# Optimization experiments

Hardware: AMD Instinct MI355X
Metric: run time of the kernel (lower is better)

## Reference

```python
import jax, jax.numpy as jnp
import numpy as np


def conv1x1(x, w, b):
    # x: [B, Cin, D, H, W], w: [Cout, Cin], b: [Cout]
    return jnp.einsum('bcdhw,oc->bodhw', x, w) + b[None, :, None, None, None]


def setup_inputs() -> dict:
    key = jax.random.key(0)
    ks = jax.random.split(key, 9)
    B, C, D, H, W = 2, 64, 16, 16, 16
    Cc = 64          # context_dim
    C8 = C // 8      # inner attention dim
    s = 0.05
    return {
        'x': jax.random.normal(ks[0], (B, C, D, H, W), jnp.float32),
        'context': jax.random.normal(ks[1], (B, Cc, D, H, W), jnp.float32),
        'Wq': jax.random.normal(ks[2], (C8, C), jnp.float32) * s,
        'bq': jax.random.normal(ks[3], (C8,), jnp.float32) * s,
        'Wk': jax.random.normal(ks[4], (C8, Cc), jnp.float32) * s,
        'bk': jax.random.normal(ks[5], (C8,), jnp.float32) * s,
        'Wv': jax.random.normal(ks[6], (C, Cc), jnp.float32) * s,
        'bv': jax.random.normal(ks[7], (C,), jnp.float32) * s,
        'gamma': jax.random.normal(ks[8], (1,), jnp.float32) * s,
    }


def reference(x, context, Wq, bq, Wk, bk, Wv, bv, gamma):
    B, C, D, H, W = x.shape
    N = D * H * W
    q = conv1x1(x, Wq, bq).reshape(B, -1, N)        # [B, C/8, N]
    k = conv1x1(context, Wk, bk).reshape(B, -1, N)  # [B, C/8, N]
    v = conv1x1(context, Wv, bv).reshape(B, C, N)   # [B, C, N]
    # energy[b, n, m] = q[:, :, n] . k[:, :, m]  (no scaling, as in source)
    energy = jnp.einsum('bcn,bcm->bnm', q, k)       # [B, N, N]
    attn = jax.nn.softmax(energy, axis=-1)
    # out = v @ attn^T : out[b, c, n] = sum_m v[b, c, m] * attn[b, n, m]
    out = jnp.einsum('bcm,bnm->bcn', v, attn).reshape(B, C, D, H, W)
    return gamma[0] * out + x
```

## Files before the change

kernel.cpp:

```cpp
#include <hip/hip_runtime.h>

#define NTOK 4096

typedef __attribute__((ext_vector_type(8))) short short8;
typedef __attribute__((ext_vector_type(4))) float f32x4;
typedef __attribute__((ext_vector_type(4))) unsigned int uint4v;

__device__ __forceinline__ unsigned short f2bf(float f) {
    unsigned u = __float_as_uint(f);
    u += 0x7fffu + ((u >> 16) & 1u);
    return (unsigned short)(u >> 16);
}

__device__ __forceinline__ float bf2f(unsigned short h) {
    return __uint_as_float((unsigned)h << 16);
}

__device__ __forceinline__ unsigned int pk2(float lo, float hi) {
    return __builtin_amdgcn_perm(__float_as_uint(hi), __float_as_uint(lo), 0x07060302u);
}

__global__ __launch_bounds__(256) void proj(
    const float* __restrict__ x, const float* __restrict__ ctx,
    const float* __restrict__ Wq, const float* __restrict__ bq,
    const float* __restrict__ Wk, const float* __restrict__ bk,
    const float* __restrict__ Wv, const float* __restrict__ bv,
    unsigned short* __restrict__ qbf, unsigned short* __restrict__ kbf,
    unsigned short* __restrict__ vtp)
{
    __shared__ float sW[16 * 64];
    __shared__ float sB[16];
    int tid  = threadIdx.x;
    int ogrp = blockIdx.z;
    int b    = blockIdx.y;
    int n0   = blockIdx.x * 64;

    if (ogrp == 0) {
        for (int i = tid; i < 1024; i += 256)
            sW[i] = (i < 512) ? Wq[i] : Wk[i - 512];
        if (tid < 16) sB[tid] = (tid < 8) ? bq[tid] : bk[tid - 8];
    } else {
        for (int i = tid; i < 1024; i += 256)
            sW[i] = Wv[(ogrp - 1) * 1024 + i];
        if (tid < 16) sB[tid] = bv[(ogrp - 1) * 16 + tid];
    }
    __syncthreads();

    int nn   = tid & 63;
    int osub = tid >> 6;
    const float* inp = (ogrp == 0 && osub < 2) ? x : ctx;
    const float* ip  = inp + (size_t)b * 64 * NTOK + n0 + nn;

    float a0 = sB[osub * 4 + 0], a1 = sB[osub * 4 + 1];
    float a2 = sB[osub * 4 + 2], a3 = sB[osub * 4 + 3];
#pragma unroll 16
    for (int c = 0; c < 64; ++c) {
        float val = ip[(size_t)c * NTOK];
        a0 += sW[(osub * 4 + 0) * 64 + c] * val;
        a1 += sW[(osub * 4 + 1) * 64 + c] * val;
        a2 += sW[(osub * 4 + 2) * 64 + c] * val;
        a3 += sW[(osub * 4 + 3) * 64 + c] * val;
    }
    float av[4] = {a0, a1, a2, a3};

    if (ogrp == 0) {
        bool isq = osub < 2;
        float sc = isq ? 1.4426950408889634f : 1.0f;
        unsigned short* dst = isq ? qbf : kbf;
        int half = osub & 1;
        ushort4 pk = {f2bf(av[0] * sc), f2bf(av[1] * sc), f2bf(av[2] * sc), f2bf(av[3] * sc)};
        *(ushort4*)&dst[((size_t)b * NTOK + n0 + nn) * 8 + half * 4] = pk;
    } else {
        int cbase = (ogrp - 1) * 16 + osub * 4;
        int m   = n0 + nn;
        int T   = m >> 5;
        int mm  = m & 31;
        int p   = ((mm >> 2) & 3) * 8 + (mm >> 4) * 4 + (mm & 3);
        int qd  = p >> 3, j2 = p & 7;
        int ctv = cbase >> 4;
        unsigned short* vB = vtp + (size_t)b * 64 * NTOK
                           + ((size_t)T * 4 + ctv) * 512;
#pragma unroll
        for (int jj = 0; jj < 4; ++jj) {
            int lanev = ((cbase + jj) & 15) + 16 * qd;
            vB[lanev * 8 + j2] = f2bf(av[jj]);
        }
    }
}

__global__ __launch_bounds__(256, 2) void attn8(
    const unsigned short* __restrict__ qbf, const unsigned short* __restrict__ kbf,
    const unsigned short* __restrict__ vtp,
    unsigned short* __restrict__ partO, float* __restrict__ partL)
{
    __shared__ float sOc[4][16][68];
    __shared__ float sL[4][64];

    int tid  = threadIdx.x;
    int w    = tid >> 6, lane = tid & 63;
    int n    = lane & 15, quad = lane >> 4;
    int nt   = blockIdx.x;
    int b    = blockIdx.y;
    int qz   = blockIdx.z;
    int n0   = nt * 64;

    const f32x4 z4 = {0.f, 0.f, 0.f, 0.f};
    const short8 z8 = {0, 0, 0, 0, 0, 0, 0, 0};

    short8 bq[4];
#pragma unroll
    for (int g = 0; g < 4; ++g)
        bq[g] = (quad == 0)
            ? *(const short8*)&qbf[((size_t)b * NTOK + n0 + g * 16 + n) * 8]
            : z8;

    const unsigned short* kb = kbf + (size_t)b * NTOK * 8;
    const unsigned short* vb = vtp + (size_t)b * 64 * NTOK;
    int mwbase = qz * 512 + w * 128;

    f32x4 acc[4][4];
#pragma unroll
    for (int g = 0; g < 4; ++g)
#pragma unroll
        for (int ct = 0; ct < 4; ++ct) acc[g][ct] = z4;
    float lsum[4] = {0.f, 0.f, 0.f, 0.f};

    for (int h = 0; h < 2; ++h) {
        int m0 = mwbase + h * 64;
        int Tb = m0 >> 5;

        short8 kf0 = (quad == 0) ? *(const short8*)&kb[(size_t)(m0 + 0 * 16 + n) * 8] : z8;
        short8 kf1 = (quad == 0) ? *(const short8*)&kb[(size_t)(m0 + 1 * 16 + n) * 8] : z8;
        short8 kf2 = (quad == 0) ? *(const short8*)&kb[(size_t)(m0 + 2 * 16 + n) * 8] : z8;
        short8 kf3 = (quad == 0) ? *(const short8*)&kb[(size_t)(m0 + 3 * 16 + n) * 8] : z8;

        short8 af[2][4];
#pragma unroll
        for (int s = 0; s < 2; ++s)
#pragma unroll
            for (int ct = 0; ct < 4; ++ct)
                af[s][ct] = *(const short8*)&vb[(((size_t)(Tb + s) * 4 + ct) * 64 + lane) * 8];

#pragma unroll
        for (int g = 0; g < 4; ++g) {
            f32x4 sa0 = __builtin_amdgcn_mfma_f32_16x16x32_bf16(kf0, bq[g], z4, 0, 0, 0);
            f32x4 sa1 = __builtin_amdgcn_mfma_f32_16x16x32_bf16(kf1, bq[g], z4, 0, 0, 0);
            f32x4 sa2 = __builtin_amdgcn_mfma_f32_16x16x32_bf16(kf2, bq[g], z4, 0, 0, 0);
            f32x4 sa3 = __builtin_amdgcn_mfma_f32_16x16x32_bf16(kf3, bq[g], z4, 0, 0, 0);

            float e00 = __builtin_amdgcn_exp2f(sa0[0]), e01 = __builtin_amdgcn_exp2f(sa0[1]);
            float e02 = __builtin_amdgcn_exp2f(sa0[2]), e03 = __builtin_amdgcn_exp2f(sa0[3]);
            float e10 = __builtin_amdgcn_exp2f(sa1[0]), e11 = __builtin_amdgcn_exp2f(sa1[1]);
            float e12 = __builtin_amdgcn_exp2f(sa1[2]), e13 = __builtin_amdgcn_exp2f(sa1[3]);
            float e20 = __builtin_amdgcn_exp2f(sa2[0]), e21 = __builtin_amdgcn_exp2f(sa2[1]);
            float e22 = __builtin_amdgcn_exp2f(sa2[2]), e23 = __builtin_amdgcn_exp2f(sa2[3]);
            float e30 = __builtin_amdgcn_exp2f(sa3[0]), e31 = __builtin_amdgcn_exp2f(sa3[1]);
            float e32 = __builtin_amdgcn_exp2f(sa3[2]), e33 = __builtin_amdgcn_exp2f(sa3[3]);
            lsum[g] += ((e00 + e01) + (e02 + e03)) + ((e10 + e11) + (e12 + e13))
                     + ((e20 + e21) + (e22 + e23)) + ((e30 + e31) + (e32 + e33));

            uint4v t0, t1;
            t0[0] = pk2(e00, e01); t0[1] = pk2(e02, e03);
            t0[2] = pk2(e10, e11); t0[3] = pk2(e12, e13);
            t1[0] = pk2(e20, e21); t1[1] = pk2(e22, e23);
            t1[2] = pk2(e30, e31); t1[3] = pk2(e32, e33);
            short8 pf0 = __builtin_bit_cast(short8, t0);
            short8 pf1 = __builtin_bit_cast(short8, t1);

            acc[g][0] = __builtin_amdgcn_mfma_f32_16x16x32_bf16(af[0][0], pf0, acc[g][0], 0, 0, 0);
            acc[g][1] = __builtin_amdgcn_mfma_f32_16x16x32_bf16(af[0][1], pf0, acc[g][1], 0, 0, 0);
            acc[g][2] = __builtin_amdgcn_mfma_f32_16x16x32_bf16(af[0][2], pf0, acc[g][2], 0, 0, 0);
            acc[g][3] = __builtin_amdgcn_mfma_f32_16x16x32_bf16(af[0][3], pf0, acc[g][3], 0, 0, 0);
            acc[g][0] = __builtin_amdgcn_mfma_f32_16x16x32_bf16(af[1][0], pf1, acc[g][0], 0, 0, 0);
            acc[g][1] = __builtin_amdgcn_mfma_f32_16x16x32_bf16(af[1][1], pf1, acc[g][1], 0, 0, 0);
            acc[g][2] = __builtin_amdgcn_mfma_f32_16x16x32_bf16(af[1][2], pf1, acc[g][2], 0, 0, 0);
            acc[g][3] = __builtin_amdgcn_mfma_f32_16x16x32_bf16(af[1][3], pf1, acc[g][3], 0, 0, 0);
        }
    }

#pragma unroll
    for (int g = 0; g < 4; ++g) {
        float l = lsum[g];
        l += __shfl_xor(l, 16);
        l += __shfl_xor(l, 32);
        if (lane < 16) sL[w][g * 16 + n] = l;
    }

    unsigned short* pO = partO + ((size_t)((b * 64 + nt) * 8 + qz)) * 4096;
    float*          pL = partL + ((size_t)((b * 64 + nt) * 8 + qz)) * 64;

#pragma unroll
    for (int ct = 0; ct < 4; ++ct) {
        if (ct) __syncthreads();
#pragma unroll
        for (int g = 0; g < 4; ++g)
#pragma unroll
            for (int r = 0; r < 4; ++r)
                sOc[w][quad * 4 + r][g * 16 + n] = acc[g][ct][r];
        __syncthreads();
        for (int i = tid; i < 1024; i += 256) {
            int c16 = i >> 6, nn2 = i & 63;
            float s = sOc[0][c16][nn2] + sOc[1][c16][nn2]
                    + sOc[2][c16][nn2] + sOc[3][c16][nn2];
            pO[ct * 1024 + i] = f2bf(s);
        }
    }
    if (tid < 64)
        pL[tid] = sL[0][tid] + sL[1][tid] + sL[2][tid] + sL[3][tid];
}

__global__ __launch_bounds__(256) void mergeq(
    const unsigned short* __restrict__ partO, const float* __restrict__ partL,
    const float* __restrict__ x, const float* __restrict__ gamma,
    float* __restrict__ out)
{
    int tid = threadIdx.x;
    int nt4 = blockIdx.x;
    int b   = blockIdx.y;
    int c   = tid >> 2;
    int j   = tid & 3;
    int nt  = nt4 >> 2;
    int ns  = (nt4 & 3) * 16 + j * 4;

    const unsigned short* pOb = partO + ((size_t)((b * 64 + nt) * 8)) * 4096;
    const float*          pLb = partL + ((size_t)((b * 64 + nt) * 8)) * 64;
    float g = gamma[0];

    float4 o = {0.f, 0.f, 0.f, 0.f};
    float4 L = {0.f, 0.f, 0.f, 0.f};
#pragma unroll
    for (int qz = 0; qz < 8; ++qz) {
        ushort4 ov = *(const ushort4*)&pOb[qz * 4096 + c * 64 + ns];
        float4  lv = *(const float4*)&pLb[qz * 64 + ns];
        o.x += bf2f(ov.x); o.y += bf2f(ov.y);
        o.z += bf2f(ov.z); o.w += bf2f(ov.w);
        L.x += lv.x; L.y += lv.y; L.z += lv.z; L.w += lv.w;
    }
    size_t ob = ((size_t)b * 64 + c) * NTOK + (size_t)nt4 * 16 + j * 4;
    float4 xv = *(const float4*)&x[ob];
    float4 res;
    res.x = g * (o.x / L.x) + xv.x;
    res.y = g * (o.y / L.y) + xv.y;
    res.z = g * (o.z / L.z) + xv.z;
    res.w = g * (o.w / L.w) + xv.w;
    *(float4*)&out[ob] = res;
}

extern "C" void kernel_launch(void* const* d_in, const int* in_sizes, int n_in,
                              void* d_out, int out_size, void* d_ws, size_t ws_size,
                              hipStream_t stream) {
    const float* x     = (const float*)d_in[0];
    const float* ctx   = (const float*)d_in[1];
    const float* Wq    = (const float*)d_in[2];
    const float* bq    = (const float*)d_in[3];
    const float* Wk    = (const float*)d_in[4];
    const float* bk    = (const float*)d_in[5];
    const float* Wv    = (const float*)d_in[6];
    const float* bv    = (const float*)d_in[7];
    const float* gamma = (const float*)d_in[8];
    float* out = (float*)d_out;

    unsigned short* qbf   = (unsigned short*)d_ws;
    unsigned short* kbf   = qbf + 2 * NTOK * 8;
    unsigned short* vtp   = kbf + 2 * NTOK * 8;
    unsigned short* partO = vtp + 2 * 64 * NTOK;
    float*          partL = (float*)(partO + (size_t)2 * 64 * 8 * 4096);

    proj<<<dim3(64, 2, 5), 256, 0, stream>>>(x, ctx, Wq, bq, Wk, bk, Wv, bv, qbf, kbf, vtp);
    attn8<<<dim3(NTOK / 64, 2, 8), 256, 0, stream>>>(qbf, kbf, vtp, partO, partL);
    mergeq<<<dim3(NTOK / 16, 2), 256, 0, stream>>>(partO, partL, x, gamma, out);
}
```

Before: 95.73 us.

## Split attention work by query group per wave, drop LDS cross-wave reduction

Each wave in the attention kernel now owns one 16-query group and walks all 512 keys of the block's key chunk. Before, each wave handled a quarter of the keys for all 64 queries. Per-wave partial outputs and row sums are written straight to global memory, which removes the shared-memory staging, the cross-wave summation and the __syncthreads barriers. Accumulator registers shrink, so the launch bound is raised to 4 blocks per SIMD for more occupancy. In exchange, every wave now loads all K and V fragments itself, giving four times the per-wave global/L2 traffic for K/V, and the output stores are scattered 2-byte writes.

After: 109.8 us. 1.15x slower.

```diff
diff --git a/kernel.cpp b/kernel.cpp
--- a/kernel.cpp
+++ b/kernel.cpp
@@ -88,14 +88,11 @@
     }
 }
 
-__global__ __launch_bounds__(256, 2) void attn8(
+__global__ __launch_bounds__(256, 4) void attn8(
     const unsigned short* __restrict__ qbf, const unsigned short* __restrict__ kbf,
     const unsigned short* __restrict__ vtp,
     unsigned short* __restrict__ partO, float* __restrict__ partL)
 {
-    __shared__ float sOc[4][16][68];
-    __shared__ float sL[4][64];
-
     int tid  = threadIdx.x;
     int w    = tid >> 6, lane = tid & 63;
     int n    = lane & 15, quad = lane >> 4;
@@ -107,26 +104,19 @@
     const f32x4 z4 = {0.f, 0.f, 0.f, 0.f};
     const short8 z8 = {0, 0, 0, 0, 0, 0, 0, 0};
 
-    short8 bq[4];
-#pragma unroll
-    for (int g = 0; g < 4; ++g)
-        bq[g] = (quad == 0)
-            ? *(const short8*)&qbf[((size_t)b * NTOK + n0 + g * 16 + n) * 8]
-            : z8;
+    short8 bqf = (quad == 0)
+        ? *(const short8*)&qbf[((size_t)b * NTOK + n0 + w * 16 + n) * 8]
+        : z8;
 
     const unsigned short* kb = kbf + (size_t)b * NTOK * 8;
     const unsigned short* vb = vtp + (size_t)b * 64 * NTOK;
-    int mwbase = qz * 512 + w * 128;
-
-    f32x4 acc[4][4];
-#pragma unroll
-    for (int g = 0; g < 4; ++g)
-#pragma unroll
-        for (int ct = 0; ct < 4; ++ct) acc[g][ct] = z4;
-    float lsum[4] = {0.f, 0.f, 0.f, 0.f};
-
-    for (int h = 0; h < 2; ++h) {
-        int m0 = mwbase + h * 64;
+    int mqbase = qz * 512;
+
+    f32x4 acc[4] = {z4, z4, z4, z4};
+    float lsum = 0.f;
+
+    for (int h = 0; h < 8; ++h) {
+        int m0 = mqbase + h * 64;
         int Tb = m0 >> 5;
 
         short8 kf0 = (quad == 0) ? *(const short8*)&kb[(size_t)(m0 + 0 * 16 + n) * 8] : z8;
@@ -141,72 +131,54 @@
             for (int ct = 0; ct < 4; ++ct)
                 af[s][ct] = *(const short8*)&vb[(((size_t)(Tb + s) * 4 + ct) * 64 + lane) * 8];
 
-#pragma unroll
-        for (int g = 0; g < 4; ++g) {
-            f32x4 sa0 = __builtin_amdgcn_mfma_f32_16x16x32_bf16(kf0, bq[g], z4, 0, 0, 0);
-            f32x4 sa1 = __builtin_amdgcn_mfma_f32_16x16x32_bf16(kf1, bq[g], z4, 0, 0, 0);
-            f32x4 sa2 = __builtin_amdgcn_mfma_f32_16x16x32_bf16(kf2, bq[g], z4, 0, 0, 0);
-            f32x4 sa3 = __builtin_amdgcn_mfma_f32_16x16x32_bf16(kf3, bq[g], z4, 0, 0, 0);
-
-            float e00 = __builtin_amdgcn_exp2f(sa0[0]), e01 = __builtin_amdgcn_exp2f(sa0[1]);
-            float e02 = __builtin_amdgcn_exp2f(sa0[2]), e03 = __builtin_amdgcn_exp2f(sa0[3]);
-            float e10 = __builtin_amdgcn_exp2f(sa1[0]), e11 = __builtin_amdgcn_exp2f(sa1[1]);
-            float e12 = __builtin_amdgcn_exp2f(sa1[2]), e13 = __builtin_amdgcn_exp2f(sa1[3]);
-            float e20 = __builtin_amdgcn_exp2f(sa2[0]), e21 = __builtin_amdgcn_exp2f(sa2[1]);
-            float e22 = __builtin_amdgcn_exp2f(sa2[2]), e23 = __builtin_amdgcn_exp2f(sa2[3]);
-            float e30 = __builtin_amdgcn_exp2f(sa3[0]), e31 = __builtin_amdgcn_exp2f(sa3[1]);
-            float e32 = __builtin_amdgcn_exp2f(sa3[2]), e33 = __builtin_amdgcn_exp2f(sa3[3]);
-            lsum[g] += ((e00 + e01) + (e02 + e03)) + ((e10 + e11) + (e12 + e13))
-                     + ((e20 + e21) + (e22 + e23)) + ((e30 + e31) + (e32 + e33));
-
-            uint4v t0, t1;
-            t0[0] = pk2(e00, e01); t0[1] = pk2(e02, e03);
-            t0[2] = pk2(e10, e11); t0[3] = pk2(e12, e13);
-            t1[0] = pk2(e20, e21); t1[1] = pk2(e22, e23);
-            t1[2] = pk2(e30, e31); t1[3] = pk2(e32, e33);
-            short8 pf0 = __builtin_bit_cast(short8, t0);
-            short8 pf1 = __builtin_bit_cast(short8, t1);
-
-            acc[g][0] = __builtin_amdgcn_mfma_f32_16x16x32_bf16(af[0][0], pf0, acc[g][0], 0, 0, 0);
-            acc[g][1] = __builtin_amdgcn_mfma_f32_16x16x32_bf16(af[0][1], pf0, acc[g][1], 0, 0, 0);
-            acc[g][2] = __builtin_amdgcn_mfma_f32_16x16x32_bf16(af[0][2], pf0, acc[g][2], 0, 0, 0);
-            acc[g][3] = __builtin_amdgcn_mfma_f32_16x16x32_bf16(af[0][3], pf0, acc[g][3], 0, 0, 0);
-            acc[g][0] = __builtin_amdgcn_mfma_f32_16x16x32_bf16(af[1][0], pf1, acc[g][0], 0, 0, 0);
-            acc[g][1] = __builtin_amdgcn_mfma_f32_16x16x32_bf16(af[1][1], pf1, acc[g][1], 0, 0, 0);
-            acc[g][2] = __builtin_amdgcn_mfma_f32_16x16x32_bf16(af[1][2], pf1, acc[g][2], 0, 0, 0);
-            acc[g][3] = __builtin_amdgcn_mfma_f32_16x16x32_bf16(af[1][3], pf1, acc[g][3], 0, 0, 0);
-        }
-    }
-
-#pragma unroll
-    for (int g = 0; g < 4; ++g) {
-        float l = lsum[g];
-        l += __shfl_xor(l, 16);
-        l += __shfl_xor(l, 32);
-        if (lane < 16) sL[w][g * 16 + n] = l;
-    }
+        f32x4 sa0 = __builtin_amdgcn_mfma_f32_16x16x32_bf16(kf0, bqf, z4, 0, 0, 0);
+        f32x4 sa1 = __builtin_amdgcn_mfma_f32_16x16x32_bf16(kf1, bqf, z4, 0, 0, 0);
+        f32x4 sa2 = __builtin_amdgcn_mfma_f32_16x16x32_bf16(kf2, bqf, z4, 0, 0, 0);
+        f32x4 sa3 = __builtin_amdgcn_mfma_f32_16x16x32_bf16(kf3, bqf, z4, 0, 0, 0);
+
+        float e00 = __builtin_amdgcn_exp2f(sa0[0]), e01 = __builtin_amdgcn_exp2f(sa0[1]);
+        float e02 = __builtin_amdgcn_exp2f(sa0[2]), e03 = __builtin_amdgcn_exp2f(sa0[3]);
+        float e10 = __builtin_amdgcn_exp2f(sa1[0]), e11 = __builtin_amdgcn_exp2f(sa1[1]);
+        float e12 = __builtin_amdgcn_exp2f(sa1[2]), e13 = __builtin_amdgcn_exp2f(sa1[3]);
+        float e20 = __builtin_amdgcn_exp2f(sa2[0]), e21 = __builtin_amdgcn_exp2f(sa2[1]);
+        float e22 = __builtin_amdgcn_exp2f(sa2[2]), e23 = __builtin_amdgcn_exp2f(sa2[3]);
+        float e30 = __builtin_amdgcn_exp2f(sa3[0]), e31 = __builtin_amdgcn_exp2f(sa3[1]);
+        float e32 = __builtin_amdgcn_exp2f(sa3[2]), e33 = __builtin_amdgcn_exp2f(sa3[3]);
+        lsum += ((e00 + e01) + (e02 + e03)) + ((e10 + e11) + (e12 + e13))
+              + ((e20 + e21) + (e22 + e23)) + ((e30 + e31) + (e32 + e33));
+
+        uint4v t0, t1;
+        t0[0] = pk2(e00, e01); t0[1] = pk2(e02, e03);
+        t0[2] = pk2(e10, e11); t0[3] = pk2(e12, e13);
+        t1[0] = pk2(e20, e21); t1[1] = pk2(e22, e23);
+        t1[2] = pk2(e30, e31); t1[3] = pk2(e32, e33);
+        short8 pf0 = __builtin_bit_cast(short8, t0);
+        short8 pf1 = __builtin_bit_cast(short8, t1);
+
+        acc[0] = __builtin_amdgcn_mfma_f32_16x16x32_bf16(af[0][0], pf0, acc[0], 0, 0, 0);
+        acc[1] = __builtin_amdgcn_mfma_f32_16x16x32_bf16(af[0][1], pf0, acc[1], 0, 0, 0);
+        acc[2] = __builtin_amdgcn_mfma_f32_16x16x32_bf16(af[0][2], pf0, acc[2], 0, 0, 0);
+        acc[3] = __builtin_amdgcn_mfma_f32_16x16x32_bf16(af[0][3], pf0, acc[3], 0, 0, 0);
+        acc[0] = __builtin_amdgcn_mfma_f32_16x16x32_bf16(af[1][0], pf1, acc[0], 0, 0, 0);
+        acc[1] = __builtin_amdgcn_mfma_f32_16x16x32_bf16(af[1][1], pf1, acc[1], 0, 0, 0);
+        acc[2] = __builtin_amdgcn_mfma_f32_16x16x32_bf16(af[1][2], pf1, acc[2], 0, 0, 0);
+        acc[3] = __builtin_amdgcn_mfma_f32_16x16x32_bf16(af[1][3], pf1, acc[3], 0, 0, 0);
+    }
+
+    float l = lsum;
+    l += __shfl_xor(l, 16);
+    l += __shfl_xor(l, 32);
 
     unsigned short* pO = partO + ((size_t)((b * 64 + nt) * 8 + qz)) * 4096;
     float*          pL = partL + ((size_t)((b * 64 + nt) * 8 + qz)) * 64;
 
-#pragma unroll
-    for (int ct = 0; ct < 4; ++ct) {
-        if (ct) __syncthreads();
-#pragma unroll
-        for (int g = 0; g < 4; ++g)
-#pragma unroll
-            for (int r = 0; r < 4; ++r)
-                sOc[w][quad * 4 + r][g * 16 + n] = acc[g][ct][r];
-        __syncthreads();
-        for (int i = tid; i < 1024; i += 256) {
-            int c16 = i >> 6, nn2 = i & 63;
-            float s = sOc[0][c16][nn2] + sOc[1][c16][nn2]
-                    + sOc[2][c16][nn2] + sOc[3][c16][nn2];
-            pO[ct * 1024 + i] = f2bf(s);
-        }
-    }
-    if (tid < 64)
-        pL[tid] = sL[0][tid] + sL[1][tid] + sL[2][tid] + sL[3][tid];
+    if (lane < 16) pL[w * 16 + lane] = l;
+
+#pragma unroll
+    for (int ct = 0; ct < 4; ++ct)
+#pragma unroll
+        for (int r = 0; r < 4; ++r)
+            pO[ct * 1024 + (quad * 4 + r) * 64 + w * 16 + n] = f2bf(acc[ct][r]);
 }
 
 __global__ __launch_bounds__(256) void mergeq(
```
